# Kernel tuning notes

Hardware: AMD Instinct MI355X
Metric: run time of the kernel (lower is better)

Reference implementation:

```python
import jax, jax.numpy as jnp
import numpy as np

N = 50000          # nodes
E = 800000         # edges (avg degree 16)
D = 64             # node_embedding_size
H = 64             # hidden_channels (heads=1, out_channels=H)
DE = 32            # edge_embedding_size


def _transformer_conv(x, src, dst, edge_attr,
                      wq, bq, wk, bk, wv, bv, we, ws, bs, n_nodes):
    # PyG TransformerConv, heads=1, concat=True, root_weight=True, edge_dim set.
    q = x @ wq + bq                      # [N, H]
    k = x @ wk + bk                      # [N, H]
    v = x @ wv + bv                      # [N, H]
    e = edge_attr @ we                   # [E, H]  (lin_edge has no bias)
    ke = k[src] + e                      # [E, H]
    score = jnp.sum(q[dst] * ke, axis=-1) / jnp.sqrt(jnp.asarray(ke.shape[-1], x.dtype))  # [E]
    # segment softmax over incoming edges of each dst node
    smax = jax.ops.segment_max(score, dst, num_segments=n_nodes)   # [N]
    a = jnp.exp(score - smax[dst])                                  # [E]
    denom = jax.ops.segment_sum(a, dst, num_segments=n_nodes)      # [N]
    alpha = a / denom[dst]                                          # [E]
    msg = alpha[:, None] * (v[src] + e)                             # [E, H]
    out = jax.ops.segment_sum(msg, dst, num_segments=n_nodes)      # [N, H]
    out = out + x @ ws + bs                                         # root skip (lin_skip)
    return out


def setup_inputs() -> dict:
    key = jax.random.key(0)
    ks = jax.random.split(key, 24)
    def g(i, shape, scale):
        return jax.random.normal(ks[i], shape, dtype=jnp.float32) * scale
    inp = {
        "x": g(0, (N, D), 1.0),
        "edge_index": jax.random.randint(ks[1], (2, E), 0, N, dtype=jnp.int64),
        "edge_attr": g(2, (E, DE), 1.0),
        # layer 1: in=D -> out=H
        "q1_w": g(3, (D, H), D ** -0.5), "q1_b": jnp.zeros((H,), jnp.float32),
        "k1_w": g(4, (D, H), D ** -0.5), "k1_b": jnp.zeros((H,), jnp.float32),
        "v1_w": g(5, (D, H), D ** -0.5), "v1_b": jnp.zeros((H,), jnp.float32),
        "e1_w": g(6, (DE, H), DE ** -0.5),
        "s1_w": g(7, (D, H), D ** -0.5), "s1_b": jnp.zeros((H,), jnp.float32),
        # layer 2: in=H -> out=H
        "q2_w": g(8, (H, H), H ** -0.5), "q2_b": jnp.zeros((H,), jnp.float32),
        "k2_w": g(9, (H, H), H ** -0.5), "k2_b": jnp.zeros((H,), jnp.float32),
        "v2_w": g(10, (H, H), H ** -0.5), "v2_b": jnp.zeros((H,), jnp.float32),
        "e2_w": g(11, (DE, H), DE ** -0.5),
        "s2_w": g(12, (H, H), H ** -0.5), "s2_b": jnp.zeros((H,), jnp.float32),
        # skip_linear: 2*H -> D
        "skip_w": g(13, (2 * H, D), (2 * H) ** -0.5),
        "skip_b": jnp.zeros((D,), jnp.float32),
    }
    return inp


def reference(x, edge_index, edge_attr,
              q1_w, q1_b, k1_w, k1_b, v1_w, v1_b, e1_w, s1_w, s1_b,
              q2_w, q2_b, k2_w, k2_b, v2_w, v2_b, e2_w, s2_w, s2_b,
              skip_w, skip_b):
    src, dst = edge_index[0], edge_index[1]
    n = x.shape[0]
    h1 = jax.nn.relu(_transformer_conv(x, src, dst, edge_attr,
                                       q1_w, q1_b, k1_w, k1_b, v1_w, v1_b,
                                       e1_w, s1_w, s1_b, n))
    h2 = jax.nn.relu(_transformer_conv(h1, src, dst, edge_attr,
                                       q2_w, q2_b, k2_w, k2_b, v2_w, v2_b,
                                       e2_w, s2_w, s2_b, n))
    skip_xs = jnp.concatenate([h1, h2], axis=-1)     # [N, 2H]
    return jax.nn.relu(skip_xs @ skip_w + skip_b)     # [N, D]
```

## Files before the change

kernel.cpp:

```cpp
#include <hip/hip_runtime.h>

#define DIM 64
#define DEA 32

__device__ __forceinline__ unsigned short f2bf(float f) {
    const unsigned u = __float_as_uint(f);
    return (unsigned short)((u + 0x7FFFu + ((u >> 16) & 1u)) >> 16);
}
__device__ __forceinline__ float bf2f(unsigned short h) {
    return __uint_as_float(((unsigned)h) << 16);
}

__global__ __launch_bounds__(256) void wqe_prep_kernel(
    const float* __restrict__ wq1, const float* __restrict__ bq1, const float* __restrict__ we1,
    const float* __restrict__ wq2, const float* __restrict__ bq2, const float* __restrict__ we2,
    float* __restrict__ w1out, float* __restrict__ b1out,
    float* __restrict__ w2out, float* __restrict__ b2out)
{
    const float* wq = blockIdx.x ? wq2 : wq1;
    const float* bq = blockIdx.x ? bq2 : bq1;
    const float* we = blockIdx.x ? we2 : we1;
    float* wout = blockIdx.x ? w2out : w1out;
    float* bout = blockIdx.x ? b2out : b1out;

    __shared__ float lq[64 * 64];
    __shared__ float lweT[64 * 33];
    const int tid = threadIdx.x;
    {
        const float4* s4 = (const float4*)wq;
        float4* d4 = (float4*)lq;
        #pragma unroll
        for (int i = 0; i < 4; ++i) d4[tid + i * 256] = s4[tid + i * 256];
        const float4* e4 = (const float4*)we;
        #pragma unroll
        for (int t = 0; t < 2; ++t) {
            const int f = tid + t * 256;
            const int j = f >> 4;
            const int o4 = (f & 15) * 4;
            const float4 v = e4[f];
            lweT[(o4 + 0) * 33 + j] = v.x;
            lweT[(o4 + 1) * 33 + j] = v.y;
            lweT[(o4 + 2) * 33 + j] = v.z;
            lweT[(o4 + 3) * 33 + j] = v.w;
        }
    }
    __syncthreads();
    const int j = tid & 31;
    const int c0 = (tid >> 5) * 8;
    for (int c = c0; c < c0 + 8; ++c) {
        float acc = 0.f;
        #pragma unroll 8
        for (int o = 0; o < 64; ++o) acc = fmaf(lq[c * 64 + o], lweT[o * 33 + j], acc);
        wout[c * 32 + j] = acc;
    }
    if (tid < 32) {
        float acc = 0.f;
        #pragma unroll 8
        for (int o = 0; o < 64; ++o) acc = fmaf(bq[o], lweT[o * 33 + tid], acc);
        bout[tid] = acc;
    }
}

__global__ __launch_bounds__(256) void node_lin_kernel(
    const float* __restrict__ x,
    const float* __restrict__ wq, const float* __restrict__ bq,
    const float* __restrict__ wk, const float* __restrict__ bk,
    const float* __restrict__ wv, const float* __restrict__ bv,
    const float* __restrict__ wsk, const float* __restrict__ bsk,
    const float* __restrict__ wqe_w, const float* __restrict__ bqe,
    float* __restrict__ q, unsigned short* __restrict__ kvb,
    float* __restrict__ agg, float* __restrict__ qwe, int n_nodes)
{
    __shared__ float lw[16 * 256];
    __shared__ float lxT[64 * 36];
    __shared__ float lwqe[64 * 32];
    const int tid = threadIdx.x;
    const int base = blockIdx.x * 32;

    {
        #pragma unroll
        for (int t = 0; t < 2; ++t) {
            const int f = tid + t * 256;
            const int node = f >> 4;
            const int c4 = (f & 15) * 4;
            const int n = base + node;
            float4 val = make_float4(0.f, 0.f, 0.f, 0.f);
            if (n < n_nodes) val = *(const float4*)&x[(size_t)n * DIM + c4];
            lxT[(c4 + 0) * 36 + node] = val.x;
            lxT[(c4 + 1) * 36 + node] = val.y;
            lxT[(c4 + 2) * 36 + node] = val.z;
            lxT[(c4 + 3) * 36 + node] = val.w;
        }
        const float4* s4 = (const float4*)wqe_w;
        float4* d4 = (float4*)lwqe;
        d4[tid] = s4[tid];
        d4[tid + 256] = s4[tid + 256];
    }

    const int m = tid >> 6;
    const int oc = tid & 63;
    const float* wsrc = (m == 0) ? wq : (m == 1) ? wk : (m == 2) ? wv : wsk;
    const float bias = ((m == 0) ? bq : (m == 1) ? bk : (m == 2) ? bv : bsk)[oc];

    float acc[32];
    #pragma unroll
    for (int r = 0; r < 32; ++r) acc[r] = 0.f;

    for (int kc = 0; kc < 4; ++kc) {
        __syncthreads();
        #pragma unroll
        for (int i = 0; i < 4; ++i) {
            const int f = oc + i * 64;
            const int kk = f >> 4;
            const int c4 = (f & 15) * 4;
            const float4 w4 = *(const float4*)&wsrc[(size_t)(kc * 16 + kk) * DIM + c4];
            *(float4*)&lw[kk * 256 + m * 64 + c4] = w4;
        }
        __syncthreads();
        #pragma unroll
        for (int kk = 0; kk < 16; ++kk) {
            const float wv_ = lw[kk * 256 + tid];
            const float* xrow = &lxT[(kc * 16 + kk) * 36];
            #pragma unroll
            for (int r4 = 0; r4 < 8; ++r4) {
                const float4 xv = *(const float4*)&xrow[r4 * 4];
                acc[r4 * 4 + 0] = fmaf(xv.x, wv_, acc[r4 * 4 + 0]);
                acc[r4 * 4 + 1] = fmaf(xv.y, wv_, acc[r4 * 4 + 1]);
                acc[r4 * 4 + 2] = fmaf(xv.z, wv_, acc[r4 * 4 + 2]);
                acc[r4 * 4 + 3] = fmaf(xv.w, wv_, acc[r4 * 4 + 3]);
            }
        }
    }

    #pragma unroll
    for (int r = 0; r < 32; ++r) {
        const int n = base + r;
        if (n < n_nodes) {
            const float val = acc[r] + bias;
            if (m == 0)      q[(size_t)n * DIM + oc]            = val;
            else if (m == 1) kvb[(size_t)n * 128 + oc]          = f2bf(val);
            else if (m == 2) kvb[(size_t)n * 128 + 64 + oc]     = f2bf(val);
            else             agg[(size_t)n * DIM + oc]          = val;
        }
    }

    {
        const int j = tid & 31;
        const int r0 = (tid >> 5) * 4;
        float a0 = 0.f, a1 = 0.f, a2 = 0.f, a3 = 0.f;
        #pragma unroll 8
        for (int c = 0; c < DIM; ++c) {
            const float wv_ = lwqe[c * 32 + j];
            const float4 xv = *(const float4*)&lxT[c * 36 + r0];
            a0 = fmaf(xv.x, wv_, a0);
            a1 = fmaf(xv.y, wv_, a1);
            a2 = fmaf(xv.z, wv_, a2);
            a3 = fmaf(xv.w, wv_, a3);
        }
        const float bb = bqe[j];
        const float av[4] = {a0 + bb, a1 + bb, a2 + bb, a3 + bb};
        #pragma unroll
        for (int i = 0; i < 4; ++i) {
            const int n = base + r0 + i;
            if (n < n_nodes) qwe[(size_t)n * DEA + j] = av[i];
        }
    }
}

__global__ __launch_bounds__(256) void hist_kernel(
    const int* __restrict__ dst, int* __restrict__ counts, int n_edges, int n_nodes)
{
    const int eid = blockIdx.x * 256 + threadIdx.x;
    if (eid >= n_edges) return;
    int d = dst[eid];
    d = (d < 0) ? 0 : ((d >= n_nodes) ? n_nodes - 1 : d);
    atomicAdd(&counts[d], 1);
}

__global__ __launch_bounds__(256) void scan_pass1_kernel(
    const int* __restrict__ counts, int* __restrict__ row_ptr,
    int* __restrict__ blksum, int n)
{
    const int tid = threadIdx.x;
    const int lane = tid & 63;
    const int base = blockIdx.x * 1024 + tid * 4;
    int c0 = 0, c1 = 0, c2 = 0, c3 = 0;
    if (base + 3 < n) {
        const int4 v = *(const int4*)&counts[base];
        c0 = v.x; c1 = v.y; c2 = v.z; c3 = v.w;
    } else {
        if (base + 0 < n) c0 = counts[base + 0];
        if (base + 1 < n) c1 = counts[base + 1];
        if (base + 2 < n) c2 = counts[base + 2];
        if (base + 3 < n) c3 = counts[base + 3];
    }
    const int tsum = c0 + c1 + c2 + c3;
    int incl = tsum;
    #pragma unroll
    for (int off = 1; off < 64; off <<= 1) {
        const int t = __shfl_up(incl, off, 64);
        if (lane >= off) incl += t;
    }
    __shared__ int wsum[4];
    const int wv = tid >> 6;
    if (lane == 63) wsum[wv] = incl;
    __syncthreads();
    int woff = 0;
    #pragma unroll
    for (int i = 0; i < 4; ++i) if (i < wv) woff += wsum[i];
    const int excl = woff + incl - tsum;
    if (base + 3 < n) {
        int4 o;
        o.x = excl; o.y = excl + c0; o.z = excl + c0 + c1; o.w = excl + c0 + c1 + c2;
        *(int4*)&row_ptr[base] = o;
    } else {
        if (base + 0 < n) row_ptr[base + 0] = excl;
        if (base + 1 < n) row_ptr[base + 1] = excl + c0;
        if (base + 2 < n) row_ptr[base + 2] = excl + c0 + c1;
        if (base + 3 < n) row_ptr[base + 3] = excl + c0 + c1 + c2;
    }
    if (tid == 255) blksum[blockIdx.x] = woff + incl;
}

__global__ __launch_bounds__(64) void scan_pass2_kernel(
    const int* __restrict__ blksum, int* __restrict__ blkoff,
    int* __restrict__ row_ptr, int nb, int n)
{
    const int lane = threadIdx.x;
    int carry = 0;
    for (int base = 0; base < nb; base += 64) {
        const int idx = base + lane;
        const int v = (idx < nb) ? blksum[idx] : 0;
        int incl = v;
        #pragma unroll
        for (int off = 1; off < 64; off <<= 1) {
            const int t = __shfl_up(incl, off, 64);
            if (lane >= off) incl += t;
        }
        if (idx < nb) blkoff[idx] = carry + incl - v;
        carry += __shfl(incl, 63, 64);
    }
    if (lane == 0) row_ptr[n] = carry;
}

__global__ __launch_bounds__(256) void scan_pass3_kernel(
    int* __restrict__ row_ptr, int* __restrict__ cursor,
    const int* __restrict__ blkoff, int n)
{
    const int base = blockIdx.x * 1024 + threadIdx.x * 4;
    const int off = blkoff[blockIdx.x];
    if (base + 3 < n) {
        int4 v = *(const int4*)&row_ptr[base];
        v.x += off; v.y += off; v.z += off; v.w += off;
        *(int4*)&row_ptr[base] = v;
        *(int4*)&cursor[base]  = v;
    } else {
        #pragma unroll
        for (int i = 0; i < 4; ++i) {
            if (base + i < n) {
                const int v = row_ptr[base + i] + off;
                row_ptr[base + i] = v;
                cursor[base + i]  = v;
            }
        }
    }
}

__global__ __launch_bounds__(256) void scatter_kernel(
    const int* __restrict__ dst, const int* __restrict__ src,
    int* __restrict__ cursor, int2* __restrict__ pair, int n_edges, int n_nodes)
{
    const int eid = blockIdx.x * 256 + threadIdx.x;
    if (eid >= n_edges) return;
    int d = dst[eid];
    d = (d < 0) ? 0 : ((d >= n_nodes) ? n_nodes - 1 : d);
    int s = src[eid];
    s = (s < 0) ? 0 : ((s >= n_nodes) ? n_nodes - 1 : s);
    const int pos = atomicAdd(&cursor[d], 1);
    pair[pos] = make_int2(eid, s);
}

__global__ __launch_bounds__(256) void fused_edge_kernel(
    const float* __restrict__ q, const float* __restrict__ qwe,
    const unsigned short* __restrict__ kvb, const float* __restrict__ ea,
    const float* __restrict__ we, const float* __restrict__ aggskip,
    const int* __restrict__ row_ptr, const int2* __restrict__ pair,
    float* __restrict__ h_out, int n_nodes)
{
    __shared__ float lw[DEA * DIM];
    const int tid = threadIdx.x;
    {
        const float4* s4 = (const float4*)we;
        float4* d4 = (float4*)lw;
        d4[tid] = s4[tid];
        d4[tid + 256] = s4[tid + 256];
    }
    __syncthreads();

    const int wave = tid >> 6;
    const int lane = tid & 63;
    const int g = lane >> 4;
    const int j = lane & 15;
    const int node = blockIdx.x * 4 + wave;
    if (node >= n_nodes) return;

    const float4 q4   = *(const float4*)&q[(size_t)node * DIM + j * 4];
    const float2 qwe2 = *(const float2*)&qwe[(size_t)node * DEA + j * 2];
    const int beg = row_ptr[node], end = row_ptr[node + 1];

    float m = -3.0e38f, l = 0.f;
    float4 msg = make_float4(0.f, 0.f, 0.f, 0.f);
    float2 sea = make_float2(0.f, 0.f);

    if (beg < end) {
        int2 pr = pair[(beg + g < end) ? (beg + g) : (end - 1)];
        for (int i0 = beg; i0 < end; i0 += 4) {
            const bool act = (i0 + g) < end;
            const int eid = pr.x;
            const int s   = pr.y;
            const unsigned short* kvp = &kvb[(size_t)s * 128];
            const ushort4 kraw = *(const ushort4*)&kvp[j * 4];
            const ushort4 vraw = *(const ushort4*)&kvp[64 + j * 4];
            const float2 ea2 = *(const float2*)&ea[(size_t)eid * DEA + j * 2];
            const int inext = i0 + 4 + g;
            if (inext < end) pr = pair[inext];

            const float4 k4 = make_float4(bf2f(kraw.x), bf2f(kraw.y), bf2f(kraw.z), bf2f(kraw.w));
            const float4 v4 = make_float4(bf2f(vraw.x), bf2f(vraw.y), bf2f(vraw.z), bf2f(vraw.w));

            float t = fmaf(q4.x, k4.x, qwe2.x * ea2.x);
            t = fmaf(q4.y, k4.y, t);
            t = fmaf(q4.z, k4.z, t);
            t = fmaf(q4.w, k4.w, t);
            t = fmaf(qwe2.y, ea2.y, t);
            t += __shfl_xor(t, 1, 64);
            t += __shfl_xor(t, 2, 64);
            t += __shfl_xor(t, 4, 64);
            t += __shfl_xor(t, 8, 64);
            const float score = act ? t * 0.125f : -3.0e38f;

            const float mn = fmaxf(m, score);
            const float p  = act ? __expf(score - mn) : 0.f;
            const float sc = __expf(m - mn);
            l = l * sc + p;
            msg.x = fmaf(p, v4.x, msg.x * sc);
            msg.y = fmaf(p, v4.y, msg.y * sc);
            msg.z = fmaf(p, v4.z, msg.z * sc);
            msg.w = fmaf(p, v4.w, msg.w * sc);
            sea.x = fmaf(p, ea2.x, sea.x * sc);
            sea.y = fmaf(p, ea2.y, sea.y * sc);
            m = mn;
        }
    }

    #pragma unroll
    for (int off = 16; off <= 32; off <<= 1) {
        const float m2 = __shfl_xor(m, off, 64);
        const float l2 = __shfl_xor(l, off, 64);
        float4 msg2;
        msg2.x = __shfl_xor(msg.x, off, 64);
        msg2.y = __shfl_xor(msg.y, off, 64);
        msg2.z = __shfl_xor(msg.z, off, 64);
        msg2.w = __shfl_xor(msg.w, off, 64);
        float2 sea2;
        sea2.x = __shfl_xor(sea.x, off, 64);
        sea2.y = __shfl_xor(sea.y, off, 64);
        const float mn = fmaxf(m, m2);
        const float s1 = __expf(m - mn);
        const float s2 = __expf(m2 - mn);
        l = l * s1 + l2 * s2;
        msg.x = msg.x * s1 + msg2.x * s2;
        msg.y = msg.y * s1 + msg2.y * s2;
        msg.z = msg.z * s1 + msg2.z * s2;
        msg.w = msg.w * s1 + msg2.w * s2;
        sea.x = sea.x * s1 + sea2.x * s2;
        sea.y = sea.y * s1 + sea2.y * s2;
        m = mn;
    }

    const float4* lw4 = (const float4*)lw;
    float4 e4 = make_float4(0.f, 0.f, 0.f, 0.f);
    #pragma unroll
    for (int tt = 0; tt < 16; ++tt) {
        const float sx = __shfl(sea.x, tt, 64);
        const float sy = __shfl(sea.y, tt, 64);
        const float4 w0 = lw4[(2 * tt) * 16 + j];
        const float4 w1 = lw4[(2 * tt + 1) * 16 + j];
        e4.x = fmaf(sx, w0.x, fmaf(sy, w1.x, e4.x));
        e4.y = fmaf(sx, w0.y, fmaf(sy, w1.y, e4.y));
        e4.z = fmaf(sx, w0.z, fmaf(sy, w1.z, e4.z));
        e4.w = fmaf(sx, w0.w, fmaf(sy, w1.w, e4.w));
    }

    if (lane < 16) {
        const float inv = (l > 0.f) ? (1.f / l) : 0.f;
        const float4 sk = *(const float4*)&aggskip[(size_t)node * DIM + j * 4];
        float4 o;
        o.x = fmaxf(fmaf(msg.x + e4.x, inv, sk.x), 0.f);
        o.y = fmaxf(fmaf(msg.y + e4.y, inv, sk.y), 0.f);
        o.z = fmaxf(fmaf(msg.z + e4.z, inv, sk.z), 0.f);
        o.w = fmaxf(fmaf(msg.w + e4.w, inv, sk.w), 0.f);
        *(float4*)&h_out[(size_t)node * DIM + j * 4] = o;
    }
}

__global__ __launch_bounds__(256) void final_kernel(
    const float* __restrict__ h1, const float* __restrict__ h2,
    const float* __restrict__ w, const float* __restrict__ b,
    float* __restrict__ out, int n_nodes)
{
    __shared__ float lw[128 * DIM];
    __shared__ float lx[16][128];
    const int tid = threadIdx.x;
    {
        const float4* s4 = (const float4*)w;
        float4* d4 = (float4*)lw;
        #pragma unroll
        for (int i = 0; i < 8; ++i) d4[tid + i * 256] = s4[tid + i * 256];
    }
    const int base = blockIdx.x * 16;
    {
        #pragma unroll
        for (int t = 0; t < 2; ++t) {
            const int f = tid + t * 256;
            const int r = f >> 5;
            const int cf = f & 31;
            const int n = base + r;
            float4 val = make_float4(0.f, 0.f, 0.f, 0.f);
            if (n < n_nodes) {
                if (cf < 16) val = *(const float4*)&h1[(size_t)n * DIM + cf * 4];
                else         val = *(const float4*)&h2[(size_t)n * DIM + (cf - 16) * 4];
            }
            *(float4*)&lx[r][cf * 4] = val;
        }
    }
    __syncthreads();

    const int oc = tid & 63;
    const int nl = tid >> 6;
    float acc[4] = {0, 0, 0, 0};
    #pragma unroll 8
    for (int kk = 0; kk < 128; ++kk) {
        const float wv = lw[kk * DIM + oc];
        #pragma unroll
        for (int r = 0; r < 4; ++r)
            acc[r] = fmaf(lx[nl * 4 + r][kk], wv, acc[r]);
    }
    const float bv = b[oc];
    #pragma unroll
    for (int r = 0; r < 4; ++r) {
        const int n = base + nl * 4 + r;
        if (n < n_nodes) out[(size_t)n * DIM + oc] = fmaxf(acc[r] + bv, 0.f);
    }
}

extern "C" void kernel_launch(void* const* d_in, const int* in_sizes, int n_in,
                              void* d_out, int out_size, void* d_ws, size_t ws_size,
                              hipStream_t stream)
{
    const float* x     = (const float*)d_in[0];
    const int*   ei    = (const int*)d_in[1];
    const float* eattr = (const float*)d_in[2];
    const float *q1w = (const float*)d_in[3],  *q1b = (const float*)d_in[4];
    const float *k1w = (const float*)d_in[5],  *k1b = (const float*)d_in[6];
    const float *v1w = (const float*)d_in[7],  *v1b = (const float*)d_in[8];
    const float *e1w = (const float*)d_in[9];
    const float *s1w = (const float*)d_in[10], *s1b = (const float*)d_in[11];
    const float *q2w = (const float*)d_in[12], *q2b = (const float*)d_in[13];
    const float *k2w = (const float*)d_in[14], *k2b = (const float*)d_in[15];
    const float *v2w = (const float*)d_in[16], *v2b = (const float*)d_in[17];
    const float *e2w = (const float*)d_in[18];
    const float *s2w = (const float*)d_in[19], *s2b = (const float*)d_in[20];
    const float *skw = (const float*)d_in[21], *skb = (const float*)d_in[22];

    const int N = in_sizes[0] / DIM;
    const int E = in_sizes[1] / 2;
    const int* src = ei;
    const int* dst = ei + E;

    float* ws = (float*)d_ws;
    const size_t nf = (size_t)N * DIM;
    float* q    = ws;
    unsigned short* kvb = (unsigned short*)(q + nf);
    float* agg  = q + 2 * nf;
    float* h1   = agg + nf;
    float* h2   = h1 + nf;
    float* qwe  = h2 + nf;
    int2* pair    = (int2*)(qwe + (size_t)DEA * N);
    int* cursor   = (int*)(pair + E);
    int* row_ptr  = cursor + ((N + 3) & ~3);
    const int nb  = (N + 1023) / 1024;
    int* blksum   = row_ptr + ((N + 4) & ~3);
    int* blkoff   = blksum + ((nb + 3) & ~3);
    float* wqeW1  = (float*)(blkoff + ((nb + 3) & ~3));
    float* bqe1   = wqeW1 + 64 * 32;
    float* wqeW2  = bqe1 + 32;
    float* bqe2   = wqeW2 + 64 * 32;

    const int nblk = (N + 31) / 32;
    const int eblk = (E + 255) / 256;
    const int fblk = (N + 3) / 4;
    const int finblk = (N + 15) / 16;

    hipMemsetAsync(cursor, 0, (size_t)N * sizeof(int), stream);
    hist_kernel<<<eblk, 256, 0, stream>>>(dst, cursor, E, N);
    scan_pass1_kernel<<<nb, 256, 0, stream>>>(cursor, row_ptr, blksum, N);
    scan_pass2_kernel<<<1, 64, 0, stream>>>(blksum, blkoff, row_ptr, nb, N);
    scan_pass3_kernel<<<nb, 256, 0, stream>>>(row_ptr, cursor, blkoff, N);
    scatter_kernel<<<eblk, 256, 0, stream>>>(dst, src, cursor, pair, E, N);
    wqe_prep_kernel<<<2, 256, 0, stream>>>(q1w, q1b, e1w, q2w, q2b, e2w,
                                           wqeW1, bqe1, wqeW2, bqe2);

    node_lin_kernel<<<nblk, 256, 0, stream>>>(x, q1w, q1b, k1w, k1b, v1w, v1b,
                                              s1w, s1b, wqeW1, bqe1,
                                              q, kvb, agg, qwe, N);
    fused_edge_kernel<<<fblk, 256, 0, stream>>>(q, qwe, kvb, eattr, e1w, agg,
                                                row_ptr, pair, h1, N);

    node_lin_kernel<<<nblk, 256, 0, stream>>>(h1, q2w, q2b, k2w, k2b, v2w, v2b,
                                              s2w, s2b, wqeW2, bqe2,
                                              q, kvb, agg, qwe, N);
    fused_edge_kernel<<<fblk, 256, 0, stream>>>(q, qwe, kvb, eattr, e2w, agg,
                                                row_ptr, pair, h2, N);

    final_kernel<<<finblk, 256, 0, stream>>>(h1, h2, skw, skb, (float*)d_out, N);
}
```

Measured before the change: 360.7 us.

## Process eight edges per wave with 8-lane groups and fold score scale into q

Switches the fused edge kernel from 4 edges × 16 lanes to 8 edges × 8 lanes per iteration, loading 16-byte bf16 K/V chunks and float4 edge attributes per lane and unpacking bf16 pairs directly from 32-bit words. The 1/sqrt(H) scale is folded into q and the q·We precompute so the per-edge multiply disappears. The epilogue now goes through per-wave shared-memory staging so all 64 lanes compute the edge-weight projection and write output. This halves loop iterations for degree-16 nodes and shortens the shuffle reduction, at the cost of more registers and an extra cross-lane merge step. There is no barrier between the shared writes by g==0 lanes and the reads by other lanes, which relies on intra-wave lockstep execution.

Result: faster. 343.1 us, median of 2 (-4.9%).

```diff
diff --git a/kernel.cpp b/kernel.cpp
--- a/kernel.cpp
+++ b/kernel.cpp
@@ -7,9 +7,8 @@
     const unsigned u = __float_as_uint(f);
     return (unsigned short)((u + 0x7FFFu + ((u >> 16) & 1u)) >> 16);
 }
-__device__ __forceinline__ float bf2f(unsigned short h) {
-    return __uint_as_float(((unsigned)h) << 16);
-}
+__device__ __forceinline__ float bflo(unsigned u) { return __uint_as_float(u << 16); }
+__device__ __forceinline__ float bfhi(unsigned u) { return __uint_as_float(u & 0xFFFF0000u); }
 
 __global__ __launch_bounds__(256) void wqe_prep_kernel(
     const float* __restrict__ wq1, const float* __restrict__ bq1, const float* __restrict__ we1,
@@ -51,13 +50,13 @@
         float acc = 0.f;
         #pragma unroll 8
         for (int o = 0; o < 64; ++o) acc = fmaf(lq[c * 64 + o], lweT[o * 33 + j], acc);
-        wout[c * 32 + j] = acc;
+        wout[c * 32 + j] = acc * 0.125f;
     }
     if (tid < 32) {
         float acc = 0.f;
         #pragma unroll 8
         for (int o = 0; o < 64; ++o) acc = fmaf(bq[o], lweT[o * 33 + tid], acc);
-        bout[tid] = acc;
+        bout[tid] = acc * 0.125f;
     }
 }
 
@@ -137,7 +136,7 @@
         const int n = base + r;
         if (n < n_nodes) {
             const float val = acc[r] + bias;
-            if (m == 0)      q[(size_t)n * DIM + oc]            = val;
+            if (m == 0)      q[(size_t)n * DIM + oc]            = val * 0.125f;
             else if (m == 1) kvb[(size_t)n * 128 + oc]          = f2bf(val);
             else if (m == 2) kvb[(size_t)n * 128 + 64 + oc]     = f2bf(val);
             else             agg[(size_t)n * DIM + oc]          = val;
@@ -288,6 +287,8 @@
     float* __restrict__ h_out, int n_nodes)
 {
     __shared__ float lw[DEA * DIM];
+    __shared__ float lsea[4][36];
+    __shared__ float lmsg[4][72];
     const int tid = threadIdx.x;
     {
         const float4* s4 = (const float4*)we;
@@ -299,109 +300,108 @@
 
     const int wave = tid >> 6;
     const int lane = tid & 63;
-    const int g = lane >> 4;
-    const int j = lane & 15;
+    const int g = lane >> 3;
+    const int j = lane & 7;
     const int node = blockIdx.x * 4 + wave;
     if (node >= n_nodes) return;
 
-    const float4 q4   = *(const float4*)&q[(size_t)node * DIM + j * 4];
-    const float2 qwe2 = *(const float2*)&qwe[(size_t)node * DEA + j * 2];
+    const float4 qa  = *(const float4*)&q[(size_t)node * DIM + j * 8];
+    const float4 qb  = *(const float4*)&q[(size_t)node * DIM + j * 8 + 4];
+    const float4 qw4 = *(const float4*)&qwe[(size_t)node * DEA + j * 4];
     const int beg = row_ptr[node], end = row_ptr[node + 1];
 
     float m = -3.0e38f, l = 0.f;
-    float4 msg = make_float4(0.f, 0.f, 0.f, 0.f);
-    float2 sea = make_float2(0.f, 0.f);
+    float4 msgA = make_float4(0.f, 0.f, 0.f, 0.f);
+    float4 msgB = make_float4(0.f, 0.f, 0.f, 0.f);
+    float4 sea  = make_float4(0.f, 0.f, 0.f, 0.f);
 
     if (beg < end) {
         int2 pr = pair[(beg + g < end) ? (beg + g) : (end - 1)];
-        for (int i0 = beg; i0 < end; i0 += 4) {
+        for (int i0 = beg; i0 < end; i0 += 8) {
             const bool act = (i0 + g) < end;
             const int eid = pr.x;
             const int s   = pr.y;
             const unsigned short* kvp = &kvb[(size_t)s * 128];
-            const ushort4 kraw = *(const ushort4*)&kvp[j * 4];
-            const ushort4 vraw = *(const ushort4*)&kvp[64 + j * 4];
-            const float2 ea2 = *(const float2*)&ea[(size_t)eid * DEA + j * 2];
-            const int inext = i0 + 4 + g;
+            const uint4 kraw = *(const uint4*)&kvp[j * 8];
+            const uint4 vraw = *(const uint4*)&kvp[64 + j * 8];
+            const float4 ea4 = *(const float4*)&ea[(size_t)eid * DEA + j * 4];
+            const int inext = i0 + 8 + g;
             if (inext < end) pr = pair[inext];
 
-            const float4 k4 = make_float4(bf2f(kraw.x), bf2f(kraw.y), bf2f(kraw.z), bf2f(kraw.w));
-            const float4 v4 = make_float4(bf2f(vraw.x), bf2f(vraw.y), bf2f(vraw.z), bf2f(vraw.w));
-
-            float t = fmaf(q4.x, k4.x, qwe2.x * ea2.x);
-            t = fmaf(q4.y, k4.y, t);
-            t = fmaf(q4.z, k4.z, t);
-            t = fmaf(q4.w, k4.w, t);
-            t = fmaf(qwe2.y, ea2.y, t);
+            float t0 = fmaf(qa.x, bflo(kraw.x), qw4.x * ea4.x);
+            t0 = fmaf(qa.y, bfhi(kraw.x), t0);
+            t0 = fmaf(qa.z, bflo(kraw.y), t0);
+            t0 = fmaf(qa.w, bfhi(kraw.y), t0);
+            t0 = fmaf(qw4.z, ea4.z, t0);
+            float t1 = fmaf(qb.x, bflo(kraw.z), qw4.y * ea4.y);
+            t1 = fmaf(qb.y, bfhi(kraw.z), t1);
+            t1 = fmaf(qb.z, bflo(kraw.w), t1);
+            t1 = fmaf(qb.w, bfhi(kraw.w), t1);
+            t1 = fmaf(qw4.w, ea4.w, t1);
+            float t = t0 + t1;
             t += __shfl_xor(t, 1, 64);
             t += __shfl_xor(t, 2, 64);
             t += __shfl_xor(t, 4, 64);
-            t += __shfl_xor(t, 8, 64);
-            const float score = act ? t * 0.125f : -3.0e38f;
+            const float score = act ? t : -3.0e38f;
 
             const float mn = fmaxf(m, score);
             const float p  = act ? __expf(score - mn) : 0.f;
             const float sc = __expf(m - mn);
             l = l * sc + p;
-            msg.x = fmaf(p, v4.x, msg.x * sc);
-            msg.y = fmaf(p, v4.y, msg.y * sc);
-            msg.z = fmaf(p, v4.z, msg.z * sc);
-            msg.w = fmaf(p, v4.w, msg.w * sc);
-            sea.x = fmaf(p, ea2.x, sea.x * sc);
-            sea.y = fmaf(p, ea2.y, sea.y * sc);
+            msgA.x = fmaf(p, bflo(vraw.x), msgA.x * sc);
+            msgA.y = fmaf(p, bfhi(vraw.x), msgA.y * sc);
+            msgA.z = fmaf(p, bflo(vraw.y), msgA.z * sc);
+            msgA.w = fmaf(p, bfhi(vraw.y), msgA.w * sc);
+            msgB.x = fmaf(p, bflo(vraw.z), msgB.x * sc);
+            msgB.y = fmaf(p, bfhi(vraw.z), msgB.y * sc);
+            msgB.z = fmaf(p, bflo(vraw.w), msgB.z * sc);
+            msgB.w = fmaf(p, bfhi(vraw.w), msgB.w * sc);
+            sea.x = fmaf(p, ea4.x, sea.x * sc);
+            sea.y = fmaf(p, ea4.y, sea.y * sc);
+            sea.z = fmaf(p, ea4.z, sea.z * sc);
+            sea.w = fmaf(p, ea4.w, sea.w * sc);
             m = mn;
         }
     }
 
     #pragma unroll
-    for (int off = 16; off <= 32; off <<= 1) {
+    for (int off = 8; off <= 32; off <<= 1) {
         const float m2 = __shfl_xor(m, off, 64);
         const float l2 = __shfl_xor(l, off, 64);
-        float4 msg2;
-        msg2.x = __shfl_xor(msg.x, off, 64);
-        msg2.y = __shfl_xor(msg.y, off, 64);
-        msg2.z = __shfl_xor(msg.z, off, 64);
-        msg2.w = __shfl_xor(msg.w, off, 64);
-        float2 sea2;
-        sea2.x = __shfl_xor(sea.x, off, 64);
-        sea2.y = __shfl_xor(sea.y, off, 64);
+        float4 a2, b2, s2;
+        a2.x = __shfl_xor(msgA.x, off, 64); a2.y = __shfl_xor(msgA.y, off, 64);
+        a2.z = __shfl_xor(msgA.z, off, 64); a2.w = __shfl_xor(msgA.w, off, 64);
+        b2.x = __shfl_xor(msgB.x, off, 64); b2.y = __shfl_xor(msgB.y, off, 64);
+        b2.z = __shfl_xor(msgB.z, off, 64); b2.w = __shfl_xor(msgB.w, off, 64);
+        s2.x = __shfl_xor(sea.x, off, 64);  s2.y = __shfl_xor(sea.y, off, 64);
+        s2.z = __shfl_xor(sea.z, off, 64);  s2.w = __shfl_xor(sea.w, off, 64);
         const float mn = fmaxf(m, m2);
-        const float s1 = __expf(m - mn);
-        const float s2 = __expf(m2 - mn);
-        l = l * s1 + l2 * s2;
-        msg.x = msg.x * s1 + msg2.x * s2;
-        msg.y = msg.y * s1 + msg2.y * s2;
-        msg.z = msg.z * s1 + msg2.z * s2;
-        msg.w = msg.w * s1 + msg2.w * s2;
-        sea.x = sea.x * s1 + sea2.x * s2;
-        sea.y = sea.y * s1 + sea2.y * s2;
+        const float w1 = __expf(m - mn);
+        const float w2 = __expf(m2 - mn);
+        l = l * w1 + l2 * w2;
+        msgA.x = msgA.x * w1 + a2.x * w2; msgA.y = msgA.y * w1 + a2.y * w2;
+        msgA.z = msgA.z * w1 + a2.z * w2; msgA.w = msgA.w * w1 + a2.w * w2;
+        msgB.x = msgB.x * w1 + b2.x * w2; msgB.y = msgB.y * w1 + b2.y * w2;
+        msgB.z = msgB.z * w1 + b2.z * w2; msgB.w = msgB.w * w1 + b2.w * w2;
+        sea.x = sea.x * w1 + s2.x * w2;   sea.y = sea.y * w1 + s2.y * w2;
+        sea.z = sea.z * w1 + s2.z * w2;   sea.w = sea.w * w1 + s2.w * w2;
         m = mn;
     }
 
-    const float4* lw4 = (const float4*)lw;
-    float4 e4 = make_float4(0.f, 0.f, 0.f, 0.f);
-    #pragma unroll
-    for (int tt = 0; tt < 16; ++tt) {
-        const float sx = __shfl(sea.x, tt, 64);
-        const float sy = __shfl(sea.y, tt, 64);
-        const float4 w0 = lw4[(2 * tt) * 16 + j];
-        const float4 w1 = lw4[(2 * tt + 1) * 16 + j];
-        e4.x = fmaf(sx, w0.x, fmaf(sy, w1.x, e4.x));
-        e4.y = fmaf(sx, w0.y, fmaf(sy, w1.y, e4.y));
-        e4.z = fmaf(sx, w0.z, fmaf(sy, w1.z, e4.z));
-        e4.w = fmaf(sx, w0.w, fmaf(sy, w1.w, e4.w));
-    }
-
-    if (lane < 16) {
-        const float inv = (l > 0.f) ? (1.f / l) : 0.f;
-        const float4 sk = *(const float4*)&aggskip[(size_t)node * DIM + j * 4];
-        float4 o;
-        o.x = fmaxf(fmaf(msg.x + e4.x, inv, sk.x), 0.f);
-        o.y = fmaxf(fmaf(msg.y + e4.y, inv, sk.y), 0.f);
-        o.z = fmaxf(fmaf(msg.z + e4.z, inv, sk.z), 0.f);
-        o.w = fmaxf(fmaf(msg.w + e4.w, inv, sk.w), 0.f);
-        *(float4*)&h_out[(size_t)node * DIM + j * 4] = o;
-    }
+    if (g == 0) {
+        *(float4*)&lsea[wave][j * 4]     = sea;
+        *(float4*)&lmsg[wave][j * 8]     = msgA;
+        *(float4*)&lmsg[wave][j * 8 + 4] = msgB;
+    }
+    const float inv = (l > 0.f) ? (1.f / l) : 0.f;
+
+    float e = 0.f;
+    #pragma unroll 8
+    for (int j2 = 0; j2 < DEA; ++j2)
+        e = fmaf(lsea[wave][j2], lw[j2 * DIM + lane], e);
+    const float msgc = lmsg[wave][lane];
+    const float sk = aggskip[(size_t)node * DIM + lane];
+    h_out[(size_t)node * DIM + lane] = fmaxf(fmaf(msgc + e, inv, sk), 0.f);
 }
 
 __global__ __launch_bounds__(256) void final_kernel(
```
